# Performance work log

Measured on AMD Instinct MI355X. Metric: run time of the kernel, lower is better.

## Reference

```python
import jax, jax.numpy as jnp
from jax import lax
import numpy as np

BATCH = 131072
D_IN = 512
D_OUT = 512
ITERS = 10
THRES = 1e-6


def bjorck_orthonormalize(w, iters=ITERS, thres=THRES):
    """Order-1 Bjorck orthonormalization: W <- 1.5*W - 0.5*W (W^T W).

    Row-orthogonal if out<=in, column-orthogonal otherwise (operate on W^T).
    Early-stops when max|delta| <= thres, matching the module's tolerance.
    """
    transpose = w.shape[0] > w.shape[1]
    if transpose:
        w = w.T

    def cond(state):
        i, _, err = state
        return jnp.logical_and(i < iters, err > thres)

    def body(state):
        i, w, _ = state
        w_new = 1.5 * w - 0.5 * (w @ (w.T @ w))
        err = jnp.max(jnp.abs(w_new - w))
        return i + 1, w_new, err

    _, w, _ = lax.while_loop(
        cond, body, (jnp.array(0, jnp.int32), w, jnp.array(jnp.inf, w.dtype))
    )
    if transpose:
        w = w.T
    return w


def setup_inputs() -> dict:
    key = jax.random.key(0)
    k1, k2 = jax.random.split(key)
    inputs = jax.random.normal(k1, (BATCH, D_IN), dtype=jnp.float32)
    # scaled Gaussian so singular values lie in (0, sqrt(3)) -> Bjorck converges
    weight = jax.random.normal(k2, (D_OUT, D_IN), dtype=jnp.float32) * (0.5 / np.sqrt(D_IN))
    return {"inputs": inputs, "weight": weight}


def reference(inputs, weight):
    # training-mode forward with projection=True, inverse=False:
    # weight.data <- bjorck(weight.data); out = F.linear(inputs, weight)
    w_proj = bjorck_orthonormalize(weight)
    return inputs @ w_proj.T  # [batch, out_features]
```

## Files before the change

### kernel.cpp

```cpp
#include <hip/hip_runtime.h>


using bf16x8 = __attribute__((ext_vector_type(8))) short;
using f32x4  = __attribute__((ext_vector_type(4))) float;
using u16x8  = __attribute__((ext_vector_type(8))) unsigned short;

#define DI 512

__device__ __forceinline__ unsigned short f2bf(float f) {
  unsigned int u = __builtin_bit_cast(unsigned int, f);
  u += 0x7FFFu + ((u >> 16) & 1u);
  return (unsigned short)(u >> 16);
}
__device__ __forceinline__ float bf2f(unsigned short h) {
  unsigned int u = ((unsigned int)h) << 16;
  return __builtin_bit_cast(float, u);
}

__global__ void k_split(const float* __restrict__ W, float* __restrict__ Wm,
                        unsigned short* __restrict__ Wh, unsigned short* __restrict__ Wl,
                        unsigned short* __restrict__ WTh, unsigned short* __restrict__ WTl) {
  int idx = blockIdx.x * blockDim.x + threadIdx.x;
  int m = idx >> 9, i = idx & 511;
  float w = W[idx];
  Wm[idx] = w;
  unsigned short h  = f2bf(w);
  unsigned short lo = f2bf(w - bf2f(h));
  Wh[idx] = h; Wl[idx] = lo;
  WTh[i * DI + m] = h; WTl[i * DI + m] = lo;
}

__global__ __launch_bounds__(256) void k_mm2(
    const unsigned short* __restrict__ Ah, const unsigned short* __restrict__ Al,
    const unsigned short* __restrict__ Bh, const unsigned short* __restrict__ Bl,
    int mode,
    const float* __restrict__ Wm_in, float* __restrict__ Wm_out,
    unsigned short* __restrict__ Oh, unsigned short* __restrict__ Ol,
    unsigned short* __restrict__ OTh, unsigned short* __restrict__ OTl) {
  const int tid = threadIdx.x;
  const int l   = tid & 63;
  const int wid = (blockIdx.x << 2) | (tid >> 6);
  const int m0  = (wid >> 5) << 4;
  const int n0  = (wid & 31) << 4;

  const int ra = (m0 + (l & 15)) * DI + ((l >> 4) << 3);
  const int rb = (n0 + (l & 15)) * DI + ((l >> 4) << 3);

  f32x4 a0 = {}, a1 = {}, a2 = {}, a3 = {}, a4 = {}, a5 = {};
#pragma unroll
  for (int k0 = 0; k0 < DI; k0 += 64) {
    bf16x8 ah0 = *(const bf16x8*)&Ah[ra + k0];
    bf16x8 al0 = *(const bf16x8*)&Al[ra + k0];
    bf16x8 bh0 = *(const bf16x8*)&Bh[rb + k0];
    bf16x8 bl0 = *(const bf16x8*)&Bl[rb + k0];
    bf16x8 ah1 = *(const bf16x8*)&Ah[ra + k0 + 32];
    bf16x8 al1 = *(const bf16x8*)&Al[ra + k0 + 32];
    bf16x8 bh1 = *(const bf16x8*)&Bh[rb + k0 + 32];
    bf16x8 bl1 = *(const bf16x8*)&Bl[rb + k0 + 32];
    a0 = __builtin_amdgcn_mfma_f32_16x16x32_bf16(ah0, bh0, a0, 0, 0, 0);
    a1 = __builtin_amdgcn_mfma_f32_16x16x32_bf16(ah0, bl0, a1, 0, 0, 0);
    a2 = __builtin_amdgcn_mfma_f32_16x16x32_bf16(al0, bh0, a2, 0, 0, 0);
    a3 = __builtin_amdgcn_mfma_f32_16x16x32_bf16(ah1, bh1, a3, 0, 0, 0);
    a4 = __builtin_amdgcn_mfma_f32_16x16x32_bf16(ah1, bl1, a4, 0, 0, 0);
    a5 = __builtin_amdgcn_mfma_f32_16x16x32_bf16(al1, bh1, a5, 0, 0, 0);
  }
  f32x4 acc = (a0 + a1) + (a2 + a3) + (a4 + a5);

  const int r0 = m0 + ((l >> 4) << 2);
  const int cn = n0 + (l & 15);
#pragma unroll
  for (int r = 0; r < 4; ++r) {
    const int gm = r0 + r, gn = cn;
    const float v = acc[r];
    if (mode == 0) {
      unsigned short h = f2bf(v);
      Oh[gm * DI + gn] = h;
      Ol[gm * DI + gn] = f2bf(v - bf2f(h));
    } else {
      const float wn = 1.5f * Wm_in[gm * DI + gn] - 0.5f * v;
      Wm_out[gm * DI + gn] = wn;
      unsigned short h  = f2bf(wn);
      unsigned short lo = f2bf(wn - bf2f(h));
      Oh[gm * DI + gn] = h;   Ol[gm * DI + gn] = lo;
      OTh[gn * DI + gm] = h;  OTl[gn * DI + gm] = lo;
    }
  }
}

__global__ __launch_bounds__(256, 2) void k_big(
    const float* __restrict__ X, const unsigned short* __restrict__ Wp,
    float* __restrict__ out) {
  __shared__ unsigned short sX[64][40];
  __shared__ unsigned short sW[512][40];
  const int tid = threadIdx.x;
  const int w = tid >> 6, l = tid & 63;

  f32x4 acc[4][8] = {};

  const int xrow = tid >> 2, xoff = (tid & 3) << 3;
  const int wrow = tid >> 2, wchunk = (tid & 3) << 3;
  const int rowbase = blockIdx.x << 6;

  for (int k0 = 0; k0 < 512; k0 += 32) {
    __syncthreads();
    {
      const float* xp = &X[(rowbase + xrow) * 512 + k0 + xoff];
      f32x4 v0 = *(const f32x4*)xp;
      f32x4 v1 = *(const f32x4*)(xp + 4);
      u16x8 h;
      h[0] = f2bf(v0[0]); h[1] = f2bf(v0[1]); h[2] = f2bf(v0[2]); h[3] = f2bf(v0[3]);
      h[4] = f2bf(v1[0]); h[5] = f2bf(v1[1]); h[6] = f2bf(v1[2]); h[7] = f2bf(v1[3]);
      *(u16x8*)&sX[xrow][xoff] = h;
    }
#pragma unroll
    for (int p = 0; p < 8; ++p) {
      *(u16x8*)&sW[wrow + p * 64][wchunk] =
          *(const u16x8*)&Wp[(wrow + p * 64) * 512 + k0 + wchunk];
    }
    __syncthreads();
    const int ke = (l >> 4) << 3;
    bf16x8 a[4], b[8];
#pragma unroll
    for (int mf = 0; mf < 4; ++mf)
      a[mf] = *(const bf16x8*)&sX[(mf << 4) + (l & 15)][ke];
#pragma unroll
    for (int nf = 0; nf < 8; ++nf)
      b[nf] = *(const bf16x8*)&sW[(w << 7) + (nf << 4) + (l & 15)][ke];
#pragma unroll
    for (int mf = 0; mf < 4; ++mf)
#pragma unroll
      for (int nf = 0; nf < 8; ++nf)
        acc[mf][nf] = __builtin_amdgcn_mfma_f32_16x16x32_bf16(a[mf], b[nf], acc[mf][nf], 0, 0, 0);
  }

  const int cn = l & 15;
#pragma unroll
  for (int mf = 0; mf < 4; ++mf) {
    const int r0 = rowbase + (mf << 4) + ((l >> 4) << 2);
#pragma unroll
    for (int nf = 0; nf < 8; ++nf) {
      const int col = (w << 7) + (nf << 4) + cn;
#pragma unroll
      for (int r = 0; r < 4; ++r)
        out[(r0 + r) * 512 + col] = acc[mf][nf][r];
    }
  }
}

extern "C" void kernel_launch(void* const* d_in, const int* in_sizes, int n_in,
                              void* d_out, int out_size, void* d_ws, size_t ws_size,
                              hipStream_t stream) {
  const float* X = (const float*)d_in[0];
  const float* W = (const float*)d_in[1];
  float* out = (float*)d_out;

  char* ws = (char*)d_ws;
  size_t off = 0;
  auto carve = [&](size_t bytes) { void* p = ws + off; off += (bytes + 255) & ~(size_t)255; return p; };

  const size_t F32 = (size_t)DI * DI * 4;
  const size_t BF  = (size_t)DI * DI * 2;

  float* Wm[2];           unsigned short *Wh[2], *Wl[2], *WTh[2], *WTl[2];
  Wm[0]  = (float*)carve(F32);          Wm[1]  = (float*)carve(F32);
  Wh[0]  = (unsigned short*)carve(BF);  Wh[1]  = (unsigned short*)carve(BF);
  Wl[0]  = (unsigned short*)carve(BF);  Wl[1]  = (unsigned short*)carve(BF);
  WTh[0] = (unsigned short*)carve(BF);  WTh[1] = (unsigned short*)carve(BF);
  WTl[0] = (unsigned short*)carve(BF);  WTl[1] = (unsigned short*)carve(BF);
  unsigned short* Gh = (unsigned short*)carve(BF);
  unsigned short* Gl = (unsigned short*)carve(BF);

  k_split<<<1024, 256, 0, stream>>>(W, Wm[0], Wh[0], Wl[0], WTh[0], WTl[0]);

  int cur = 0;
  for (int it = 0; it < 10; ++it) {
    k_mm2<<<256, 256, 0, stream>>>(WTh[cur], WTl[cur], WTh[cur], WTl[cur], 0,
                                   nullptr, nullptr, Gh, Gl, nullptr, nullptr);
    const int nxt = cur ^ 1;
    k_mm2<<<256, 256, 0, stream>>>(Wh[cur], Wl[cur], Gh, Gl, 1,
                                   Wm[cur], Wm[nxt], Wh[nxt], Wl[nxt], WTh[nxt], WTl[nxt]);
    cur = nxt;
  }

  k_big<<<2048, 256, 0, stream>>>(X, Wh[cur], out);
}
```

Before: 369.8 us.

## Double-buffer big GEMM with async LDS loads, swizzle, and split-K small GEMMs

The big X·W^T kernel now double-buffers its shared-memory tiles. It stages W through global_load_lds when that builtin exists and uses an XOR-swizzled unpadded LDS layout to avoid bank conflicts. The MFMA operands are swapped so each lane writes a contiguous f32x4 to the output instead of scalar stores. Separately, the small Bjorck GEMMs are split over K across two waves and reduced through shared memory, doubling the grid to raise occupancy on the latency-bound 512x512 products. The risks are the extra reduction sync and the harder-to-check swizzle indexing used by the global-to-LDS path.

```diff
diff --git a/kernel.cpp b/kernel.cpp
--- a/kernel.cpp
+++ b/kernel.cpp
@@ -38,17 +38,21 @@
     unsigned short* __restrict__ Oh, unsigned short* __restrict__ Ol,
     unsigned short* __restrict__ OTh, unsigned short* __restrict__ OTl) {
   const int tid = threadIdx.x;
-  const int l   = tid & 63;
-  const int wid = (blockIdx.x << 2) | (tid >> 6);
-  const int m0  = (wid >> 5) << 4;
-  const int n0  = (wid & 31) << 4;
-
-  const int ra = (m0 + (l & 15)) * DI + ((l >> 4) << 3);
-  const int rb = (n0 + (l & 15)) * DI + ((l >> 4) << 3);
-
-  f32x4 a0 = {}, a1 = {}, a2 = {}, a3 = {}, a4 = {}, a5 = {};
-#pragma unroll
-  for (int k0 = 0; k0 < DI; k0 += 64) {
+  const int l = tid & 63, lw = tid >> 6;
+  const int wid = (blockIdx.x << 2) | lw;
+  const int tile = wid >> 1, half = wid & 1;
+  const int m0 = (tile >> 5) << 4, n0 = (tile & 31) << 4;
+  const int kb = half << 8;
+  const int lm = l & 15, lk = l >> 4;
+  const int ra = (m0 + lm) * DI + kb + (lk << 3);
+  const int rb = (n0 + lm) * DI + kb + (lk << 3);
+
+  __shared__ f32x4 red[2][64];
+  const int pr = lw >> 1;
+
+  f32x4 a0{}, a1{}, a2{}, a3{}, a4{}, a5{};
+#pragma unroll
+  for (int k0 = 0; k0 < 256; k0 += 64) {
     bf16x8 ah0 = *(const bf16x8*)&Ah[ra + k0];
     bf16x8 al0 = *(const bf16x8*)&Al[ra + k0];
     bf16x8 bh0 = *(const bf16x8*)&Bh[rb + k0];
@@ -66,83 +70,125 @@
   }
   f32x4 acc = (a0 + a1) + (a2 + a3) + (a4 + a5);
 
-  const int r0 = m0 + ((l >> 4) << 2);
-  const int cn = n0 + (l & 15);
-#pragma unroll
-  for (int r = 0; r < 4; ++r) {
-    const int gm = r0 + r, gn = cn;
-    const float v = acc[r];
-    if (mode == 0) {
-      unsigned short h = f2bf(v);
-      Oh[gm * DI + gn] = h;
-      Ol[gm * DI + gn] = f2bf(v - bf2f(h));
-    } else {
-      const float wn = 1.5f * Wm_in[gm * DI + gn] - 0.5f * v;
-      Wm_out[gm * DI + gn] = wn;
-      unsigned short h  = f2bf(wn);
-      unsigned short lo = f2bf(wn - bf2f(h));
-      Oh[gm * DI + gn] = h;   Ol[gm * DI + gn] = lo;
-      OTh[gn * DI + gm] = h;  OTl[gn * DI + gm] = lo;
-    }
-  }
-}
+  if (half) red[pr][l] = acc;
+  __syncthreads();
+  if (!half) {
+    acc += red[pr][l];
+    const int r0 = m0 + (lk << 2);
+    const int cn = n0 + lm;
+#pragma unroll
+    for (int r = 0; r < 4; ++r) {
+      const int gm = r0 + r, gn = cn;
+      const float v = acc[r];
+      if (mode == 0) {
+        unsigned short h = f2bf(v);
+        Oh[gm * DI + gn] = h;
+        Ol[gm * DI + gn] = f2bf(v - bf2f(h));
+      } else {
+        const float wn = 1.5f * Wm_in[gm * DI + gn] - 0.5f * v;
+        Wm_out[gm * DI + gn] = wn;
+        unsigned short h = f2bf(wn), lo = f2bf(wn - bf2f(h));
+        Oh[gm * DI + gn] = h;   Ol[gm * DI + gn] = lo;
+        OTh[gn * DI + gm] = h;  OTl[gn * DI + gm] = lo;
+      }
+    }
+  }
+}
+
+#if defined(__has_builtin)
+#if __has_builtin(__builtin_amdgcn_global_load_lds)
+#define HAVE_GLDS 1
+#endif
+#endif
+
+#ifdef HAVE_GLDS
+__device__ __forceinline__ void gl2lds16(const unsigned short* g, unsigned short* lds) {
+  __builtin_amdgcn_global_load_lds(
+      (const __attribute__((address_space(1))) void*)g,
+      (__attribute__((address_space(3))) void*)lds, 16, 0, 0);
+}
+#endif
 
 __global__ __launch_bounds__(256, 2) void k_big(
     const float* __restrict__ X, const unsigned short* __restrict__ Wp,
     float* __restrict__ out) {
-  __shared__ unsigned short sX[64][40];
-  __shared__ unsigned short sW[512][40];
+  __shared__ unsigned short sA[2][2048];
+  __shared__ unsigned short sB[2][16384];
   const int tid = threadIdx.x;
   const int w = tid >> 6, l = tid & 63;
+  const int lm = l & 15, lk = l >> 4;
+  const int ck = lk ^ ((lm >> 1) & 3);
+  const int rowbase = blockIdx.x << 6;
+
+  const int arow = tid >> 2, ac = tid & 3;
+  const int alds = (arow * 4 + (ac ^ ((arow >> 1) & 3))) * 8;
+  const float* xsrc = &X[(rowbase + arow) * DI + ac * 8];
+
+  const int brow_l = l >> 2;
+  const int bcs = (l & 3) ^ ((brow_l >> 1) & 3);
 
   f32x4 acc[4][8] = {};
 
-  const int xrow = tid >> 2, xoff = (tid & 3) << 3;
-  const int wrow = tid >> 2, wchunk = (tid & 3) << 3;
-  const int rowbase = blockIdx.x << 6;
-
-  for (int k0 = 0; k0 < 512; k0 += 32) {
+  auto stage_b = [&](int kk, int bb) {
+#pragma unroll
+    for (int ph = 0; ph < 8; ++ph) {
+      const int rowblk = ph * 64 + w * 16;
+      const unsigned short* src = &Wp[(rowblk + brow_l) * DI + (kk << 5) + bcs * 8];
+#ifdef HAVE_GLDS
+      gl2lds16(src, &sB[bb][rowblk * 32]);
+#else
+      u16x8 v = *(const u16x8*)src;
+      *(u16x8*)&sB[bb][rowblk * 32 + l * 8] = v;
+#endif
+    }
+  };
+
+  f32x4 xv0 = *(const f32x4*)xsrc;
+  f32x4 xv1 = *(const f32x4*)(xsrc + 4);
+  stage_b(0, 0);
+  {
+    u16x8 h;
+    h[0] = f2bf(xv0[0]); h[1] = f2bf(xv0[1]); h[2] = f2bf(xv0[2]); h[3] = f2bf(xv0[3]);
+    h[4] = f2bf(xv1[0]); h[5] = f2bf(xv1[1]); h[6] = f2bf(xv1[2]); h[7] = f2bf(xv1[3]);
+    *(u16x8*)&sA[0][alds] = h;
+  }
+  __syncthreads();
+
+  for (int k = 0; k < 16; ++k) {
+    const int buf = k & 1;
+    if (k < 15) {
+      xv0 = *(const f32x4*)(xsrc + ((k + 1) << 5));
+      xv1 = *(const f32x4*)(xsrc + ((k + 1) << 5) + 4);
+      stage_b(k + 1, buf ^ 1);
+    }
+    bf16x8 a[4], b[8];
+#pragma unroll
+    for (int mf = 0; mf < 4; ++mf)
+      a[mf] = *(const bf16x8*)&sA[buf][((mf * 16 + lm) * 4 + ck) * 8];
+#pragma unroll
+    for (int nf = 0; nf < 8; ++nf)
+      b[nf] = *(const bf16x8*)&sB[buf][((w * 128 + nf * 16 + lm) * 4 + ck) * 8];
+#pragma unroll
+    for (int mf = 0; mf < 4; ++mf)
+#pragma unroll
+      for (int nf = 0; nf < 8; ++nf)
+        acc[mf][nf] = __builtin_amdgcn_mfma_f32_16x16x32_bf16(b[nf], a[mf], acc[mf][nf], 0, 0, 0);
+    if (k < 15) {
+      u16x8 h;
+      h[0] = f2bf(xv0[0]); h[1] = f2bf(xv0[1]); h[2] = f2bf(xv0[2]); h[3] = f2bf(xv0[3]);
+      h[4] = f2bf(xv1[0]); h[5] = f2bf(xv1[1]); h[6] = f2bf(xv1[2]); h[7] = f2bf(xv1[3]);
+      *(u16x8*)&sA[buf ^ 1][alds] = h;
+    }
     __syncthreads();
-    {
-      const float* xp = &X[(rowbase + xrow) * 512 + k0 + xoff];
-      f32x4 v0 = *(const f32x4*)xp;
-      f32x4 v1 = *(const f32x4*)(xp + 4);
-      u16x8 h;
-      h[0] = f2bf(v0[0]); h[1] = f2bf(v0[1]); h[2] = f2bf(v0[2]); h[3] = f2bf(v0[3]);
-      h[4] = f2bf(v1[0]); h[5] = f2bf(v1[1]); h[6] = f2bf(v1[2]); h[7] = f2bf(v1[3]);
-      *(u16x8*)&sX[xrow][xoff] = h;
-    }
-#pragma unroll
-    for (int p = 0; p < 8; ++p) {
-      *(u16x8*)&sW[wrow + p * 64][wchunk] =
-          *(const u16x8*)&Wp[(wrow + p * 64) * 512 + k0 + wchunk];
-    }
-    __syncthreads();
-    const int ke = (l >> 4) << 3;
-    bf16x8 a[4], b[8];
-#pragma unroll
-    for (int mf = 0; mf < 4; ++mf)
-      a[mf] = *(const bf16x8*)&sX[(mf << 4) + (l & 15)][ke];
-#pragma unroll
-    for (int nf = 0; nf < 8; ++nf)
-      b[nf] = *(const bf16x8*)&sW[(w << 7) + (nf << 4) + (l & 15)][ke];
-#pragma unroll
-    for (int mf = 0; mf < 4; ++mf)
-#pragma unroll
-      for (int nf = 0; nf < 8; ++nf)
-        acc[mf][nf] = __builtin_amdgcn_mfma_f32_16x16x32_bf16(a[mf], b[nf], acc[mf][nf], 0, 0, 0);
-  }
-
-  const int cn = l & 15;
+  }
+
 #pragma unroll
   for (int mf = 0; mf < 4; ++mf) {
-    const int r0 = rowbase + (mf << 4) + ((l >> 4) << 2);
+    const int gm = rowbase + (mf << 4) + lm;
 #pragma unroll
     for (int nf = 0; nf < 8; ++nf) {
-      const int col = (w << 7) + (nf << 4) + cn;
-#pragma unroll
-      for (int r = 0; r < 4; ++r)
-        out[(r0 + r) * 512 + col] = acc[mf][nf][r];
+      const int gn = (w << 7) + (nf << 4) + (lk << 2);
+      *(f32x4*)&out[gm * DI + gn] = acc[mf][nf];
     }
   }
 }
@@ -174,10 +220,10 @@
 
   int cur = 0;
   for (int it = 0; it < 10; ++it) {
-    k_mm2<<<256, 256, 0, stream>>>(WTh[cur], WTl[cur], WTh[cur], WTl[cur], 0,
+    k_mm2<<<512, 256, 0, stream>>>(WTh[cur], WTl[cur], WTh[cur], WTl[cur], 0,
                                    nullptr, nullptr, Gh, Gl, nullptr, nullptr);
     const int nxt = cur ^ 1;
-    k_mm2<<<256, 256, 0, stream>>>(Wh[cur], Wl[cur], Gh, Gl, 1,
+    k_mm2<<<512, 256, 0, stream>>>(Wh[cur], Wl[cur], Gh, Gl, 1,
                                    Wm[cur], Wm[nxt], Wh[nxt], Wl[nxt], WTh[nxt], WTl[nxt]);
     cur = nxt;
   }
```

Result: slower. 391.2 us (+5.8%).
